# Optimization experiments

Measured on AMD Instinct MI355X. Metric: run time of the kernel, lower is better.

Reference implementation:

```python
import jax, jax.numpy as jnp
import numpy as np

N, H, V, K = 16384, 2048, 50257, 25  # tokens, hidden, vocab, num_noise


def setup_inputs() -> dict:
    key = jax.random.key(0)
    k_in, k_w, k_u, k_t, k_n = jax.random.split(key, 5)
    inp = jax.random.normal(k_in, (N, H), dtype=jnp.float32)
    stdv = 1.0 / np.sqrt(H)  # matches reset_parameters uniform(-stdv, stdv)
    weight = jax.random.uniform(k_w, (V, H), dtype=jnp.float32, minval=-stdv, maxval=stdv)
    bias = jnp.full((V,), -np.log(V), dtype=jnp.float32)  # bias.fill_(-log(odim))
    u = jax.random.uniform(k_u, (V,), dtype=jnp.float32)
    unigram_prob = u / jnp.sum(u)
    target = jax.random.randint(k_t, (N,), 0, V)
    noise = jax.random.randint(k_n, (K,), 0, V)  # multinomial draw externalized
    return {"input": inp, "weight": weight, "bias": bias,
            "unigram_prob": unigram_prob, "target": target, "noise": noise}


def reference(input, weight, bias, unigram_prob, target, noise):
    # NCE train mode: model scores for target word and K shared noise words.
    w_target = weight[target]                                   # [N, H] gather
    pmt = jnp.exp(jnp.einsum('nh,nh->n', input, w_target) + bias[target])  # [N]
    pnt = unigram_prob[target]                                  # [N]
    w_noise = weight[noise]                                     # [K, H] gather
    # pmn[n,k] = exp(input[n] . W[noise[k]] + b[noise[k]])  (no repeat materialization)
    pmn = jnp.exp(input @ w_noise.T + bias[noise])              # [N, K]
    pnn = jnp.broadcast_to(unigram_prob[noise], (N, K))         # [N, K]
    return pmt, pnt, pmn, pnn
```

## Files before the change

kernel.cpp:

```cpp
#include <hip/hip_runtime.h>
#include <math.h>

#define NTOK 16384
#define HDIM 2048
#define KNOI 25
#define RPW  2
#define WPB  4
#define CHUNK 256
#define NCHUNK (HDIM / CHUNK)

typedef __attribute__((address_space(3))) unsigned lds_uint;
typedef __attribute__((address_space(1))) const unsigned glob_uint;

__device__ __forceinline__ void stage16(const void* g, void* l) {
    __builtin_amdgcn_global_load_lds((glob_uint*)g, (lds_uint*)l, 16, 0, 0);
}

__global__ __launch_bounds__(256, 4) void nce_main(
    const float* __restrict__ input,
    const float* __restrict__ weight,
    const float* __restrict__ bias,
    const float* __restrict__ uni,
    const int* __restrict__ target,
    const int* __restrict__ noise,
    float* __restrict__ out)
{
    __shared__ float4 ldsn[KNOI * (CHUNK / 4)];

    float* pmt = out;
    float* pnt = out + NTOK;
    float* pmn = out + 2 * NTOK;
    float* pnn = out + 2 * NTOK + NTOK * KNOI;

    const int lane = threadIdx.x & 63;
    const int wave = threadIdx.x >> 6;
    int row0 = (blockIdx.x * WPB + wave) * RPW;
    row0 = __builtin_amdgcn_readfirstlane(row0);

    unsigned noffb[KNOI];
#pragma unroll
    for (int k = 0; k < KNOI; ++k)
        noffb[k] = (unsigned)noise[k] * (unsigned)(HDIM * 4);

    unsigned toffb[RPW], ioffb[RPW];
#pragma unroll
    for (int r = 0; r < RPW; ++r) {
        toffb[r] = (unsigned)target[row0 + r] * (unsigned)(HDIM * 4);
        ioffb[r] = (unsigned)(row0 + r) * (unsigned)(HDIM * 4);
    }

    const char* wb = (const char*)weight;
    const char* ib = (const char*)input;
    const unsigned laneoff = (unsigned)lane * 16u;

    float acc[RPW][KNOI];
    float acct[RPW];
#pragma unroll
    for (int r = 0; r < RPW; ++r) {
        acct[r] = 0.f;
#pragma unroll
        for (int k = 0; k < KNOI; ++k) acc[r][k] = 0.f;
    }

    float4 inv[RPW], tgv[RPW];
#pragma unroll
    for (int r = 0; r < RPW; ++r) {
        inv[r] = *(const float4*)(ib + ioffb[r] + laneoff);
        tgv[r] = *(const float4*)(wb + toffb[r] + laneoff);
    }

    for (int c = 0; c < NCHUNK; ++c) {
        const unsigned cb = (unsigned)c * (unsigned)(CHUNK * 4);

#pragma unroll
        for (int j = 0; j < 7; ++j) {
            const int k = j * WPB + wave;
            if (k < KNOI)
                stage16(wb + noffb[k] + cb + laneoff, &ldsn[k * (CHUNK / 4)]);
        }
        __syncthreads();

        const float4 in0 = inv[0], in1 = inv[1];
        const float4 tg0 = tgv[0], tg1 = tgv[1];
        const unsigned nb = (unsigned)((c + 1) & (NCHUNK - 1)) * (unsigned)(CHUNK * 4);
#pragma unroll
        for (int r = 0; r < RPW; ++r) {
            inv[r] = *(const float4*)(ib + ioffb[r] + nb + laneoff);
            tgv[r] = *(const float4*)(wb + toffb[r] + nb + laneoff);
        }

#pragma unroll
        for (int k = 0; k < KNOI; ++k) {
            const float4 w = ldsn[k * (CHUNK / 4) + lane];
            acc[0][k] += in0.x * w.x + in0.y * w.y + in0.z * w.z + in0.w * w.w;
            acc[1][k] += in1.x * w.x + in1.y * w.y + in1.z * w.z + in1.w * w.w;
        }
        acct[0] += in0.x * tg0.x + in0.y * tg0.y + in0.z * tg0.z + in0.w * tg0.w;
        acct[1] += in1.x * tg1.x + in1.y * tg1.y + in1.z * tg1.z + in1.w * tg1.w;

        __syncthreads();
    }

#pragma unroll
    for (int r = 0; r < RPW; ++r) {
#pragma unroll
        for (int m = 32; m >= 1; m >>= 1)
            acct[r] += __shfl_xor(acct[r], m, 64);
#pragma unroll
        for (int k = 0; k < KNOI; ++k) {
#pragma unroll
            for (int m = 32; m >= 1; m >>= 1)
                acc[r][k] += __shfl_xor(acc[r][k], m, 64);
        }
    }

#pragma unroll
    for (int r = 0; r < RPW; ++r) {
        if (lane == r) {
            const int row = row0 + r;
            const int tk = (int)(toffb[r] >> 13);
            pmt[row] = expf(acct[r] + bias[tk]);
            pnt[row] = uni[tk];
#pragma unroll
            for (int k = 0; k < KNOI; ++k) {
                const int nk = (int)(noffb[k] >> 13);
                pmn[row * KNOI + k] = expf(acc[r][k] + bias[nk]);
                pnn[row * KNOI + k] = uni[nk];
            }
        }
    }
}

extern "C" void kernel_launch(void* const* d_in, const int* in_sizes, int n_in,
                              void* d_out, int out_size, void* d_ws, size_t ws_size,
                              hipStream_t stream) {
    const float* input  = (const float*)d_in[0];
    const float* weight = (const float*)d_in[1];
    const float* bias   = (const float*)d_in[2];
    const float* uni    = (const float*)d_in[3];
    const int*   target = (const int*)d_in[4];
    const int*   noise  = (const int*)d_in[5];
    float* out = (float*)d_out;

    const dim3 grid(NTOK / (WPB * RPW));
    const dim3 block(256);
    hipLaunchKernelGGL(nce_main, grid, block, 0, stream,
                       input, weight, bias, uni, target, noise, out);
}
```

Before: 569.9 us.

## Drop LDS staging of noise rows, raise rows per wave, use transpose-reduce

Removes the LDS staging of the 25 noise weight rows and the two block barriers per chunk. Each wave now reads the noise rows straight from global memory (which should hit cache) and processes 4 rows per wave instead of 2, so each noise load feeds more FMAs. The final reduction is replaced with a butterfly that halves the vector at each shuffle stage, so each lane ends with one output sum instead of 26 full 64-lane reductions. The cost is higher register pressure (launch bounds lowered to 3 waves/SIMD), loss of the software prefetch of input and target rows, and more direct global/L2 traffic for the noise weights.

```diff
diff --git a/kernel.cpp b/kernel.cpp
--- a/kernel.cpp
+++ b/kernel.cpp
@@ -4,19 +4,12 @@
 #define NTOK 16384
 #define HDIM 2048
 #define KNOI 25
-#define RPW  2
+#define RPW  4
 #define WPB  4
 #define CHUNK 256
 #define NCHUNK (HDIM / CHUNK)
 
-typedef __attribute__((address_space(3))) unsigned lds_uint;
-typedef __attribute__((address_space(1))) const unsigned glob_uint;
-
-__device__ __forceinline__ void stage16(const void* g, void* l) {
-    __builtin_amdgcn_global_load_lds((glob_uint*)g, (lds_uint*)l, 16, 0, 0);
-}
-
-__global__ __launch_bounds__(256, 4) void nce_main(
+__global__ __launch_bounds__(256, 3) void nce_main(
     const float* __restrict__ input,
     const float* __restrict__ weight,
     const float* __restrict__ bias,
@@ -25,8 +18,6 @@
     const int* __restrict__ noise,
     float* __restrict__ out)
 {
-    __shared__ float4 ldsn[KNOI * (CHUNK / 4)];
-
     float* pmt = out;
     float* pnt = out + NTOK;
     float* pmn = out + 2 * NTOK;
@@ -62,70 +53,69 @@
         for (int k = 0; k < KNOI; ++k) acc[r][k] = 0.f;
     }
 
-    float4 inv[RPW], tgv[RPW];
-#pragma unroll
-    for (int r = 0; r < RPW; ++r) {
-        inv[r] = *(const float4*)(ib + ioffb[r] + laneoff);
-        tgv[r] = *(const float4*)(wb + toffb[r] + laneoff);
-    }
+#pragma unroll 1
+    for (int c = 0; c < NCHUNK; ++c) {
+        const unsigned cb = (unsigned)c * (unsigned)(CHUNK * 4) + laneoff;
 
-    for (int c = 0; c < NCHUNK; ++c) {
-        const unsigned cb = (unsigned)c * (unsigned)(CHUNK * 4);
-
-#pragma unroll
-        for (int j = 0; j < 7; ++j) {
-            const int k = j * WPB + wave;
-            if (k < KNOI)
-                stage16(wb + noffb[k] + cb + laneoff, &ldsn[k * (CHUNK / 4)]);
-        }
-        __syncthreads();
-
-        const float4 in0 = inv[0], in1 = inv[1];
-        const float4 tg0 = tgv[0], tg1 = tgv[1];
-        const unsigned nb = (unsigned)((c + 1) & (NCHUNK - 1)) * (unsigned)(CHUNK * 4);
+        float4 inv[RPW], tgv[RPW];
 #pragma unroll
         for (int r = 0; r < RPW; ++r) {
-            inv[r] = *(const float4*)(ib + ioffb[r] + nb + laneoff);
-            tgv[r] = *(const float4*)(wb + toffb[r] + nb + laneoff);
+            inv[r] = *(const float4*)(ib + ioffb[r] + cb);
+            tgv[r] = *(const float4*)(wb + toffb[r] + cb);
         }
 
 #pragma unroll
         for (int k = 0; k < KNOI; ++k) {
-            const float4 w = ldsn[k * (CHUNK / 4) + lane];
-            acc[0][k] += in0.x * w.x + in0.y * w.y + in0.z * w.z + in0.w * w.w;
-            acc[1][k] += in1.x * w.x + in1.y * w.y + in1.z * w.z + in1.w * w.w;
+            const float4 w = *(const float4*)(wb + noffb[k] + cb);
+#pragma unroll
+            for (int r = 0; r < RPW; ++r)
+                acc[r][k] += inv[r].x * w.x + inv[r].y * w.y
+                           + inv[r].z * w.z + inv[r].w * w.w;
         }
-        acct[0] += in0.x * tg0.x + in0.y * tg0.y + in0.z * tg0.z + in0.w * tg0.w;
-        acct[1] += in1.x * tg1.x + in1.y * tg1.y + in1.z * tg1.z + in1.w * tg1.w;
+#pragma unroll
+        for (int r = 0; r < RPW; ++r)
+            acct[r] += inv[r].x * tgv[r].x + inv[r].y * tgv[r].y
+                     + inv[r].z * tgv[r].z + inv[r].w * tgv[r].w;
+    }
 
-        __syncthreads();
-    }
+    const int m = ((lane >> 5) & 1) | (((lane >> 4) & 1) << 1)
+                | (((lane >> 3) & 1) << 2) | (((lane >> 2) & 1) << 3)
+                | (((lane >> 1) & 1) << 4);
 
 #pragma unroll
     for (int r = 0; r < RPW; ++r) {
+        float v[32];
 #pragma unroll
-        for (int m = 32; m >= 1; m >>= 1)
-            acct[r] += __shfl_xor(acct[r], m, 64);
+        for (int k = 0; k < KNOI; ++k) v[k] = acc[r][k];
+        v[KNOI] = acct[r];
 #pragma unroll
-        for (int k = 0; k < KNOI; ++k) {
-#pragma unroll
-            for (int m = 32; m >= 1; m >>= 1)
-                acc[r][k] += __shfl_xor(acc[r][k], m, 64);
-        }
-    }
+        for (int j = KNOI + 1; j < 32; ++j) v[j] = 0.f;
 
 #pragma unroll
-    for (int r = 0; r < RPW; ++r) {
-        if (lane == r) {
+        for (int s = 0; s < 5; ++s) {
+            const int h  = 32 >> s;
+            const int np = 16 >> s;
+#pragma unroll
+            for (int i = 0; i < np; ++i) {
+                const float lo = v[2 * i], hi = v[2 * i + 1];
+                const bool up = (lane & h) != 0;
+                const float send = up ? lo : hi;
+                const float recv = __shfl_xor(send, h, 64);
+                v[i] = (up ? hi : lo) + recv;
+            }
+        }
+        const float tot = v[0] + __shfl_xor(v[0], 1, 64);
+
+        if ((lane & 1) == 0) {
             const int row = row0 + r;
-            const int tk = (int)(toffb[r] >> 13);
-            pmt[row] = expf(acct[r] + bias[tk]);
-            pnt[row] = uni[tk];
-#pragma unroll
-            for (int k = 0; k < KNOI; ++k) {
-                const int nk = (int)(noffb[k] >> 13);
-                pmn[row * KNOI + k] = expf(acc[r][k] + bias[nk]);
-                pnn[row * KNOI + k] = uni[nk];
+            if (m < KNOI) {
+                const int nk = noise[m];
+                pmn[row * KNOI + m] = expf(tot + bias[nk]);
+                pnn[row * KNOI + m] = uni[nk];
+            } else if (m == KNOI) {
+                const int tk = (int)(toffb[r] >> 13);
+                pmt[row] = expf(tot + bias[tk]);
+                pnt[row] = uni[tk];
             }
         }
     }
```

Measured after the change: 1.533 ms. +169.0%, slower.

## Use transpose-reduce butterfly for 26 wave reductions and distribute epilogue across lanes

Applied to the files above, without the earlier changes.

Replaces the 26 independent full-wave xor-shuffle reductions per row (six shuffles each) with a recursive-halving butterfly. Each step exchanges half of the remaining values, so the total shuffle count drops sharply, and each lane ends up holding the sum for one output index (noise k or target). The exp, bias and unigram writes are then done in parallel by 26 lanes instead of serially by one lane. The occupancy hint also changes from launch_bounds min-blocks to amdgpu_waves_per_eu(4,4), which may shift register allocation. The padded 32-entry array and the select logic add some register pressure.

```diff
diff --git a/kernel.cpp b/kernel.cpp
--- a/kernel.cpp
+++ b/kernel.cpp
@@ -16,7 +16,9 @@
     __builtin_amdgcn_global_load_lds((glob_uint*)g, (lds_uint*)l, 16, 0, 0);
 }
 
-__global__ __launch_bounds__(256, 4) void nce_main(
+__global__ __launch_bounds__(256)
+__attribute__((amdgpu_waves_per_eu(4, 4)))
+void nce_main(
     const float* __restrict__ input,
     const float* __restrict__ weight,
     const float* __restrict__ bias,
@@ -101,31 +103,44 @@
         __syncthreads();
     }
 
-#pragma unroll
-    for (int r = 0; r < RPW; ++r) {
-#pragma unroll
-        for (int m = 32; m >= 1; m >>= 1)
-            acct[r] += __shfl_xor(acct[r], m, 64);
-#pragma unroll
-        for (int k = 0; k < KNOI; ++k) {
-#pragma unroll
-            for (int m = 32; m >= 1; m >>= 1)
-                acc[r][k] += __shfl_xor(acc[r][k], m, 64);
-        }
-    }
+    const int m = ((lane >> 5) & 1) | (((lane >> 4) & 1) << 1)
+                | (((lane >> 3) & 1) << 2) | (((lane >> 2) & 1) << 3)
+                | (((lane >> 1) & 1) << 4);
 
 #pragma unroll
     for (int r = 0; r < RPW; ++r) {
-        if (lane == r) {
+        float v[32];
+#pragma unroll
+        for (int k = 0; k < KNOI; ++k) v[k] = acc[r][k];
+        v[KNOI] = acct[r];
+#pragma unroll
+        for (int j = KNOI + 1; j < 32; ++j) v[j] = 0.f;
+
+#pragma unroll
+        for (int s = 0; s < 5; ++s) {
+            const int h  = 32 >> s;
+            const int np = 16 >> s;
+#pragma unroll
+            for (int i = 0; i < np; ++i) {
+                const float lo = v[2 * i], hi = v[2 * i + 1];
+                const bool up = (lane & h) != 0;
+                const float send = up ? lo : hi;
+                const float recv = __shfl_xor(send, h, 64);
+                v[i] = (up ? hi : lo) + recv;
+            }
+        }
+        const float tot = v[0] + __shfl_xor(v[0], 1, 64);
+
+        if ((lane & 1) == 0) {
             const int row = row0 + r;
-            const int tk = (int)(toffb[r] >> 13);
-            pmt[row] = expf(acct[r] + bias[tk]);
-            pnt[row] = uni[tk];
-#pragma unroll
-            for (int k = 0; k < KNOI; ++k) {
-                const int nk = (int)(noffb[k] >> 13);
-                pmn[row * KNOI + k] = expf(acc[r][k] + bias[nk]);
-                pnn[row * KNOI + k] = uni[nk];
+            if (m < KNOI) {
+                const int nk = noise[m];
+                pmn[row * KNOI + m] = expf(tot + bias[nk]);
+                pnn[row * KNOI + m] = uni[nk];
+            } else if (m == KNOI) {
+                const int tk = (int)(toffb[r] >> 13);
+                pmt[row] = expf(tot + bias[tk]);
+                pnt[row] = uni[tk];
             }
         }
     }
```

Measured after the change: 582.5 us. +2.2%, slower.
